# Kernel tuning notes

Hardware: AMD Instinct MI355X
Metric: run time of the kernel (lower is better)

The kernel has to match this reference:

```python
import jax, jax.numpy as jnp
import numpy as np

L, N, M = 128, 512, 256   # batch-like dim, recurrence length, feature dim (M_size1)
TK, H = 4, 8              # num_blocks, num_heads
DH = M // H
EPS = 1e-5


def setup_inputs() -> dict:
    key = jax.random.key(0)
    ks = jax.random.split(key, 8)
    s = 0.05  # scale raw-randn params for numerical stability
    return {
        "x": jax.random.normal(ks[0], (L, N, M), jnp.float32),
        "weight": jax.random.normal(ks[1], (M, M), jnp.float32) * s,
        "Wqkv": jax.random.normal(ks[2], (TK, 3, H, DH, M), jnp.float32) * s,
        "Wo": jax.random.normal(ks[3], (TK, M, M), jnp.float32) * s,
        "ln_g": jnp.ones((M,), jnp.float32),
        "ln_b": jnp.zeros((M,), jnp.float32),
        "lnz_g": jnp.ones((M,), jnp.float32),
        "lnz_b": jnp.zeros((M,), jnp.float32),
        "fc1_w": jax.random.normal(ks[4], (4 * M, M), jnp.float32) / np.float32(np.sqrt(M)),
        "fc1_b": jnp.zeros((4 * M,), jnp.float32),
        "fc2_w": jax.random.normal(ks[5], (M, 4 * M), jnp.float32) / np.float32(np.sqrt(4 * M)),
        "fc2_b": jnp.zeros((M,), jnp.float32),
    }


def _ln(x, g, b):
    mu = x.mean(-1, keepdims=True)
    var = x.var(-1, keepdims=True)  # biased variance, as torch LayerNorm
    return (x - mu) * jax.lax.rsqrt(var + EPS) * g + b


def _pos_bias(dtype):
    # bias[j, z]   = sin(j / 10000**(2z/M)) for even z
    # bias[j, z+1] = cos(j / 10000**(2z/M))
    pos = jnp.arange(N, dtype=dtype)                      # j
    z = jnp.arange(0, M, 2, dtype=dtype)                  # even indices
    ang = pos[:, None] / (10000.0 ** (2.0 * z / M))       # (N, M/2)
    return jnp.stack([jnp.sin(ang), jnp.cos(ang)], axis=-1).reshape(N, M)


def reference(x, weight, Wqkv, Wo, ln_g, ln_b, lnz_g, lnz_b, fc1_w, fc1_b, fc2_w, fc2_b):
    # savespace: (L, N, M); positional bias depends only on (j, feature)
    s = jnp.einsum('lm,ijm->ijl', weight, x) + _pos_bias(x.dtype)[None]
    inv_sqrt_dh = np.float32(1.0 / np.sqrt(DH))
    for a in range(TK):
        qkv = jnp.einsum('xhdm,ijm->xijhd', Wqkv[a], _ln(s, ln_g, ln_b))
        q, k, v = qkv[0], qkv[1], qkv[2]                  # each (L, N, H, DH)
        rsa = jnp.einsum('ijhd,ijhd->ijh', q * inv_sqrt_dh, k)
        imv = rsa[..., None] * v                           # (L, N, H, DH)
        imv = jnp.cumsum(imv, axis=1)                      # retention recurrence over j
        s = jnp.einsum('nm,ijm->ijn', Wo[a], imv.reshape(L, N, M)) + s
        s = _ln(s, lnz_g, lnz_b) + s
        h = jax.nn.gelu(s @ fc1_w.T + fc1_b, approximate=False)
        s = h @ fc2_w.T + fc2_b
    return s
```

## Files before the change

kernel.cpp:

```cpp
#include <hip/hip_runtime.h>

typedef unsigned int u32;
typedef unsigned short u16;
typedef _Float16 f16;
typedef __attribute__((ext_vector_type(8))) _Float16 f16x8;
typedef __attribute__((ext_vector_type(4))) float f32x4;
typedef __attribute__((ext_vector_type(4))) u16 u16x4;

#define L_ 128
#define N_ 512
#define M_ 256
#define TK_ 4
#define H_ 8
#define R_ (L_*N_)
#define FF_ 1024

__device__ __forceinline__ u16 f2h(float v){ f16 h=(f16)v; return __builtin_bit_cast(u16,h); }
__device__ __forceinline__ float h2f(u16 b){ return (float)__builtin_bit_cast(f16,b); }
__device__ __forceinline__ f32x4 mfmah(f16x8 a, f16x8 b, f32x4 c){
  return __builtin_amdgcn_mfma_f32_16x16x32_f16(a,b,c,0,0,0);
}
__device__ __forceinline__ float gelu_f(float x){
  float e = __expf(-1.702f*x);
  float r = __builtin_amdgcn_rcpf(e + 1.f);
  return x*r;
}


__global__ void k_bias(float* __restrict__ bias){
  int j = blockIdx.x, l = threadIdx.x;
  int t = l>>1;
  float base = expf(-0.14391156831212757f * (float)t);
  float ang = (float)j * base;
  bias[j*M_ + l] = (l&1) ? cosf(ang) : sinf(ang);
}

__global__ void k_pack(const float* __restrict__ src, u16* __restrict__ dst, int K){
  int b = blockIdx.x; int nk = K>>6; int cg = b/nk, k64 = b%nk;
  int t = threadIdx.x;
  int st = t>>6, g = (t>>4)&3, lr = t&15;
  const float* sp = src + (cg*16+lr)*K + k64*64 + st*32 + g*8;
  f16x8 hv;
  #pragma unroll
  for (int e=0;e<8;e++) hv[e] = (f16)sp[e];
  *(f16x8*)(dst + b*1024 + t*8) = hv;
}

__global__ void k_pack_qkv(const float* __restrict__ w, u16* __restrict__ dst){
  int b = blockIdx.x;
  int a = b/192; int rmn = b%192; int grp = rmn>>2, k64 = rmn&3;
  int hd = grp/6, cidx = grp%6;
  int t = threadIdx.x;
  int st = t>>6, g = (t>>4)&3, lr = t&15;
  int cl = cidx*16 + lr;
  int x = cl>>5, d = cl&31;
  const float* sp = w + (((a*3+x)*H_+hd)*32 + d)*M_ + k64*64 + st*32 + g*8;
  f16x8 hv;
  #pragma unroll
  for (int e=0;e<8;e++) hv[e] = (f16)sp[e];
  *(f16x8*)(dst + b*1024 + t*8) = hv;
}

__device__ __forceinline__ void stageA16(const u16* __restrict__ src, u16* __restrict__ Abuf,
                                         int rowbase, int tid){
  int row = tid>>3, skh = tid&7;
  int k64 = skh>>1, st = skh&1;
  int rg = row>>4, lr = row&15;
  const u16* sp = src + (rowbase+row)*M_ + k64*64 + st*32;
  u16* dp = Abuf + (k64*4+rg)*1024 + st*512 + lr*8;
  #pragma unroll
  for (int gg=0;gg<4;gg++)
    *(uint4*)(dp + gg*128) = *(const uint4*)(sp + gg*8);
}

__global__ __launch_bounds__(512) void k_init(const float* __restrict__ X, const u16* __restrict__ Wf,
    const float* __restrict__ bias, const float* __restrict__ lg, const float* __restrict__ lb,
    float* __restrict__ out, u16* __restrict__ P1){
  __shared__ __align__(16) u16 Abuf[16*1024];
  __shared__ float zs[8][64][2];
  int tid = threadIdx.x;
  int wx = tid>>6, lane = tid&63;
  int g = lane>>4, lr = lane&15;
  int lo = g*128 + lr*8;
  int rowbase = blockIdx.x*64;
  {
    int row = tid>>3, skh = tid&7;
    int k64 = skh>>1, st = skh&1;
    int rg = row>>4, slr = row&15;
    const float* sp = X + (rowbase+row)*M_ + k64*64 + st*32;
    u16* dp = Abuf + (k64*4+rg)*1024 + st*512 + slr*8;
    #pragma unroll
    for (int gg=0;gg<4;gg++){
      f16x8 hv;
      #pragma unroll
      for (int e=0;e<8;e++) hv[e] = (f16)sp[gg*8+e];
      *(f16x8*)(dp + gg*128) = hv;
    }
  }
  __syncthreads();
  f32x4 acc[4][2];
  #pragma unroll
  for (int i=0;i<4;i++){ acc[i][0]=0.f; acc[i][1]=0.f; }
  #pragma unroll
  for (int k64=0;k64<4;k64++)
    #pragma unroll
    for (int st=0;st<2;st++){
      f16x8 a[4], b[2];
      #pragma unroll
      for (int i=0;i<4;i++) a[i] = *(const f16x8*)(Abuf + (k64*4 + i)*1024 + st*512 + lo);
      #pragma unroll
      for (int j=0;j<2;j++) b[j] = *(const f16x8*)(Wf + ((wx*2+j)*4 + k64)*1024 + st*512 + lo);
      #pragma unroll
      for (int i=0;i<4;i++)
        #pragma unroll
        for (int j=0;j<2;j++) acc[i][j] = mfmah(a[i], b[j], acc[i][j]);
    }
  #pragma unroll
  for (int i=0;i<4;i++)
    #pragma unroll
    for (int j=0;j<2;j++)
      #pragma unroll
      for (int r=0;r<4;r++){
        int row = rowbase + i*16 + g*4 + r;
        int col = wx*32 + j*16 + lr;
        acc[i][j][r] += bias[(row & (N_-1))*M_ + col];
        out[row*M_ + col] = acc[i][j][r];
      }
  #pragma unroll
  for (int i=0;i<4;i++)
    #pragma unroll
    for (int r=0;r<4;r++){
      float ps = 0.f, qs = 0.f;
      #pragma unroll
      for (int j=0;j<2;j++){ float t = acc[i][j][r]; ps += t; qs += t*t; }
      ps += __shfl_xor(ps,1); qs += __shfl_xor(qs,1);
      ps += __shfl_xor(ps,2); qs += __shfl_xor(qs,2);
      ps += __shfl_xor(ps,4); qs += __shfl_xor(qs,4);
      ps += __shfl_xor(ps,8); qs += __shfl_xor(qs,8);
      if (lr == 0){
        int rowl = i*16 + g*4 + r;
        zs[wx][rowl][0] = ps;
        zs[wx][rowl][1] = qs;
      }
    }
  __syncthreads();
  #pragma unroll
  for (int i=0;i<4;i++)
    #pragma unroll
    for (int r=0;r<4;r++){
      int rowl = i*16 + g*4 + r;
      float sum=0.f, sq=0.f;
      #pragma unroll
      for (int q=0;q<8;q++){ sum += zs[q][rowl][0]; sq += zs[q][rowl][1]; }
      float mean = sum*(1.f/M_);
      float var  = sq*(1.f/M_) - mean*mean;
      float rstd = rsqrtf(var + 1e-5f);
      int row = rowbase + rowl;
      #pragma unroll
      for (int j=0;j<2;j++){
        int col = wx*32 + j*16 + lr;
        P1[row*M_ + col] = f2h((acc[i][j][r]-mean)*rstd*lg[col] + lb[col]);
      }
    }
}

__global__ __launch_bounds__(512) void k_qkv(const u16* __restrict__ P1, const u16* __restrict__ Wq,
    u16* __restrict__ imv){
  __shared__ __align__(16) u16 Abuf[16*1024];
  int tid = threadIdx.x;
  int hd = tid>>6, lane = tid&63;
  int g = lane>>4, lr = lane&15;
  int lo = g*128 + lr*8;
  int rowbase = blockIdx.x*64;
  stageA16(P1, Abuf, rowbase, tid);
  __syncthreads();
  const u16* Wb = Wq + hd*6*4096;
  const float isd = 0.17677669529663687f;
  float rsa[4][4];
  {
    f32x4 aqk[4][4];
    #pragma unroll
    for (int i=0;i<4;i++)
      #pragma unroll
      for (int c=0;c<4;c++) aqk[i][c] = 0.f;
    #pragma unroll
    for (int k64=0;k64<4;k64++)
      #pragma unroll
      for (int st=0;st<2;st++){
        f16x8 a[4];
        #pragma unroll
        for (int i=0;i<4;i++) a[i] = *(const f16x8*)(Abuf + (k64*4 + i)*1024 + st*512 + lo);
        #pragma unroll
        for (int c=0;c<4;c++){
          f16x8 b = *(const f16x8*)(Wb + (c*4 + k64)*1024 + st*512 + lo);
          #pragma unroll
          for (int i=0;i<4;i++) aqk[i][c] = mfmah(a[i], b, aqk[i][c]);
        }
      }
    #pragma unroll
    for (int i=0;i<4;i++){
      f32x4 p = aqk[i][0]*aqk[i][2] + aqk[i][1]*aqk[i][3];
      #pragma unroll
      for (int r=0;r<4;r++){
        float v = p[r];
        v += __shfl_xor(v,1); v += __shfl_xor(v,2);
        v += __shfl_xor(v,4); v += __shfl_xor(v,8);
        rsa[i][r] = v * isd;
      }
    }
  }
  f32x4 av[4][2];
  #pragma unroll
  for (int i=0;i<4;i++){ av[i][0]=0.f; av[i][1]=0.f; }
  #pragma unroll
  for (int k64=0;k64<4;k64++)
    #pragma unroll
    for (int st=0;st<2;st++){
      f16x8 a[4];
      #pragma unroll
      for (int i=0;i<4;i++) a[i] = *(const f16x8*)(Abuf + (k64*4 + i)*1024 + st*512 + lo);
      #pragma unroll
      for (int c=0;c<2;c++){
        f16x8 b = *(const f16x8*)(Wb + ((4+c)*4 + k64)*1024 + st*512 + lo);
        #pragma unroll
        for (int i=0;i<4;i++) av[i][c] = mfmah(a[i], b, av[i][c]);
      }
    }
  #pragma unroll
  for (int i=0;i<4;i++)
    #pragma unroll
    for (int r=0;r<4;r++){
      int row = rowbase + i*16 + g*4 + r;
      imv[row*M_ + hd*32 + lr]      = f2h(rsa[i][r]*av[i][0][r]);
      imv[row*M_ + hd*32 + 16 + lr] = f2h(rsa[i][r]*av[i][1][r]);
    }
}

__global__ __launch_bounds__(256) void k_scan(const u16* __restrict__ imv, u16* __restrict__ P1){
  __shared__ float tot[4][64][2];
  const u32* s32 = (const u32*)imv;
  u32* d32 = (u32*)P1;
  int bi = blockIdx.x;
  int i = bi>>1, mc = bi&1;
  int tid = threadIdx.x;
  int ml = tid&63, jc = tid>>6;
  int base = i*(N_*M_/2) + jc*128*(M_/2) + mc*64 + ml;
  float a0 = 0.f, a1 = 0.f;
  for (int jb=0;jb<128;jb+=8){
    u32 t[8];
    #pragma unroll
    for (int u=0;u<8;u++) t[u] = s32[base + (jb+u)*(M_/2)];
    #pragma unroll
    for (int u=0;u<8;u++){ a0 += h2f((u16)(t[u]&0xffff)); a1 += h2f((u16)(t[u]>>16)); }
  }
  tot[jc][ml][0] = a0; tot[jc][ml][1] = a1;
  __syncthreads();
  float p0 = 0.f, p1 = 0.f;
  #pragma unroll
  for (int q=0;q<3;q++) if (q<jc){ p0 += tot[q][ml][0]; p1 += tot[q][ml][1]; }
  a0 = p0; a1 = p1;
  for (int jb=0;jb<128;jb+=8){
    u32 t[8];
    #pragma unroll
    for (int u=0;u<8;u++) t[u] = s32[base + (jb+u)*(M_/2)];
    #pragma unroll
    for (int u=0;u<8;u++){
      a0 += h2f((u16)(t[u]&0xffff));
      a1 += h2f((u16)(t[u]>>16));
      d32[base + (jb+u)*(M_/2)] = (u32)f2h(a0) | ((u32)f2h(a1)<<16);
    }
  }
}

__global__ __launch_bounds__(512) void k_wo(u16* __restrict__ P1, const u16* __restrict__ Wf,
    const float* __restrict__ sold, const float* __restrict__ lg, const float* __restrict__ lb){
  __shared__ __align__(16) u16 Abuf[16*1024];
  __shared__ float zs[8][64][2];
  int tid = threadIdx.x;
  int wx = tid>>6, lane = tid&63;
  int g = lane>>4, lr = lane&15;
  int lo = g*128 + lr*8;
  int rowbase = blockIdx.x*64;
  stageA16(P1, Abuf, rowbase, tid);
  __syncthreads();
  f32x4 acc[4][2];
  #pragma unroll
  for (int i=0;i<4;i++){ acc[i][0]=0.f; acc[i][1]=0.f; }
  #pragma unroll
  for (int k64=0;k64<4;k64++)
    #pragma unroll
    for (int st=0;st<2;st++){
      f16x8 a[4], b[2];
      #pragma unroll
      for (int i=0;i<4;i++) a[i] = *(const f16x8*)(Abuf + (k64*4 + i)*1024 + st*512 + lo);
      #pragma unroll
      for (int j=0;j<2;j++) b[j] = *(const f16x8*)(Wf + ((wx*2+j)*4 + k64)*1024 + st*512 + lo);
      #pragma unroll
      for (int i=0;i<4;i++)
        #pragma unroll
        for (int j=0;j<2;j++) acc[i][j] = mfmah(a[i], b[j], acc[i][j]);
    }
  #pragma unroll
  for (int i=0;i<4;i++)
    #pragma unroll
    for (int j=0;j<2;j++)
      #pragma unroll
      for (int r=0;r<4;r++){
        int row = rowbase + i*16 + g*4 + r;
        int col = wx*32 + j*16 + lr;
        acc[i][j][r] += sold[row*M_ + col];
      }
  #pragma unroll
  for (int i=0;i<4;i++)
    #pragma unroll
    for (int r=0;r<4;r++){
      float ps = 0.f, qs = 0.f;
      #pragma unroll
      for (int j=0;j<2;j++){ float t = acc[i][j][r]; ps += t; qs += t*t; }
      ps += __shfl_xor(ps,1); qs += __shfl_xor(qs,1);
      ps += __shfl_xor(ps,2); qs += __shfl_xor(qs,2);
      ps += __shfl_xor(ps,4); qs += __shfl_xor(qs,4);
      ps += __shfl_xor(ps,8); qs += __shfl_xor(qs,8);
      if (lr == 0){
        int rowl = i*16 + g*4 + r;
        zs[wx][rowl][0] = ps;
        zs[wx][rowl][1] = qs;
      }
    }
  __syncthreads();
  #pragma unroll
  for (int i=0;i<4;i++)
    #pragma unroll
    for (int r=0;r<4;r++){
      int rowl = i*16 + g*4 + r;
      float sum=0.f, sq=0.f;
      #pragma unroll
      for (int q=0;q<8;q++){ sum += zs[q][rowl][0]; sq += zs[q][rowl][1]; }
      float mean = sum*(1.f/M_);
      float var  = sq*(1.f/M_) - mean*mean;
      float rstd = rsqrtf(var + 1e-5f);
      int row = rowbase + rowl;
      #pragma unroll
      for (int j=0;j<2;j++){
        int col = wx*32 + j*16 + lr;
        float zv = acc[i][j][r];
        P1[row*M_ + col] = f2h((zv-mean)*rstd*lg[col] + lb[col] + zv);
      }
    }
}

__global__ __launch_bounds__(512) void k_fc(u16* __restrict__ P1,
    const u16* __restrict__ W1f, const float* __restrict__ b1,
    const u16* __restrict__ W2f, const float* __restrict__ b2,
    const float* __restrict__ lg, const float* __restrict__ lb,
    float* __restrict__ out){
  __shared__ __align__(16) u16 Abuf[16*1024];
  __shared__ __align__(16) u16 Hbuf[2][64*128];
  __shared__ float zs[8][64][2];
  int tid = threadIdx.x;
  int wx = tid>>6, lane = tid&63;
  int g = lane>>4, lr = lane&15;
  int lo = g*128 + lr*8;
  int rowbase = blockIdx.x*64;
  stageA16(P1, Abuf, rowbase, tid);
  __syncthreads();
  f32x4 acc2[4][2];
  #pragma unroll
  for (int i=0;i<4;i++){ acc2[i][0]=0.f; acc2[i][1]=0.f; }
  for (int c=0;c<8;c++){
    u16* Hb = Hbuf[c&1];
    f32x4 acc1[4];
    #pragma unroll
    for (int j=0;j<4;j++) acc1[j] = 0.f;
    #pragma unroll
    for (int k64=0;k64<4;k64++)
      #pragma unroll
      for (int st=0;st<2;st++){
        f16x8 aw = *(const f16x8*)(W1f + ((c*8 + wx)*4 + k64)*1024 + st*512 + lo);
        #pragma unroll
        for (int j=0;j<4;j++){
          f16x8 bs = *(const f16x8*)(Abuf + (k64*4 + j)*1024 + st*512 + lo);
          acc1[j] = mfmah(aw, bs, acc1[j]);
        }
      }
    {
      int fl = wx*16 + g*4;
      int kc = fl>>6, kloc = fl&63;
      float4 b1v = *(const float4*)(b1 + c*128 + fl);
      float bb[4] = {b1v.x, b1v.y, b1v.z, b1v.w};
      #pragma unroll
      for (int j=0;j<4;j++){
        int row = j*16 + lr;
        u16x4 hv;
        #pragma unroll
        for (int r=0;r<4;r++)
          hv[r] = f2h(gelu_f(acc1[j][r] + bb[r]));
        int phys = ((kloc>>3) ^ row) & 7;
        *(u16x4*)(Hb + row*128 + kc*64 + phys*8 + (kloc&7)) = hv;
      }
    }
    __syncthreads();
    #pragma unroll
    for (int kcl=0;kcl<2;kcl++)
      #pragma unroll
      for (int st=0;st<2;st++){
        f16x8 ah[4], bb2[2];
        #pragma unroll
        for (int j=0;j<2;j++)
          bb2[j] = *(const f16x8*)(W2f + ((wx*2+j)*16 + c*2 + kcl)*1024 + st*512 + lo);
        #pragma unroll
        for (int i=0;i<4;i++){
          int hrow = i*16 + lr;
          int phys = (((st<<2)|g) ^ hrow) & 7;
          ah[i] = *(const f16x8*)(Hb + hrow*128 + kcl*64 + phys*8);
        }
        #pragma unroll
        for (int i=0;i<4;i++)
          #pragma unroll
          for (int j=0;j<2;j++) acc2[i][j] = mfmah(ah[i], bb2[j], acc2[i][j]);
      }
  }
  #pragma unroll
  for (int i=0;i<4;i++)
    #pragma unroll
    for (int j=0;j<2;j++)
      #pragma unroll
      for (int r=0;r<4;r++){
        int row = rowbase + i*16 + g*4 + r;
        int col = wx*32 + j*16 + lr;
        acc2[i][j][r] += b2[col];
        out[row*M_ + col] = acc2[i][j][r];
      }
  #pragma unroll
  for (int i=0;i<4;i++)
    #pragma unroll
    for (int r=0;r<4;r++){
      float ps = 0.f, qs = 0.f;
      #pragma unroll
      for (int j=0;j<2;j++){ float t = acc2[i][j][r]; ps += t; qs += t*t; }
      ps += __shfl_xor(ps,1); qs += __shfl_xor(qs,1);
      ps += __shfl_xor(ps,2); qs += __shfl_xor(qs,2);
      ps += __shfl_xor(ps,4); qs += __shfl_xor(qs,4);
      ps += __shfl_xor(ps,8); qs += __shfl_xor(qs,8);
      if (lr == 0){
        int rowl = i*16 + g*4 + r;
        zs[wx][rowl][0] = ps;
        zs[wx][rowl][1] = qs;
      }
    }
  __syncthreads();
  #pragma unroll
  for (int i=0;i<4;i++)
    #pragma unroll
    for (int r=0;r<4;r++){
      int rowl = i*16 + g*4 + r;
      float sum=0.f, sq=0.f;
      #pragma unroll
      for (int q=0;q<8;q++){ sum += zs[q][rowl][0]; sq += zs[q][rowl][1]; }
      float mean = sum*(1.f/M_);
      float var  = sq*(1.f/M_) - mean*mean;
      float rstd = rsqrtf(var + 1e-5f);
      int row = rowbase + rowl;
      #pragma unroll
      for (int j=0;j<2;j++){
        int col = wx*32 + j*16 + lr;
        P1[row*M_ + col] = f2h((acc2[i][j][r]-mean)*rstd*lg[col] + lb[col]);
      }
    }
}

extern "C" void kernel_launch(void* const* d_in, const int* in_sizes, int n_in,
                              void* d_out, int out_size, void* d_ws, size_t ws_size,
                              hipStream_t stream){
  const float* x      = (const float*)d_in[0];
  const float* weight = (const float*)d_in[1];
  const float* wqkv   = (const float*)d_in[2];
  const float* wo     = (const float*)d_in[3];
  const float* ln_g   = (const float*)d_in[4];
  const float* ln_b   = (const float*)d_in[5];
  const float* lnz_g  = (const float*)d_in[6];
  const float* lnz_b  = (const float*)d_in[7];
  const float* fc1_w  = (const float*)d_in[8];
  const float* fc1_b  = (const float*)d_in[9];
  const float* fc2_w  = (const float*)d_in[10];
  const float* fc2_b  = (const float*)d_in[11];
  float* out = (float*)d_out;
  char* ws = (char*)d_ws;
  size_t off = 0;
  u16* wqkvf   = (u16*)(ws + off); off += 1572864;
  u16* wof     = (u16*)(ws + off); off += 524288;
  u16* fc1f    = (u16*)(ws + off); off += 524288;
  u16* fc2f    = (u16*)(ws + off); off += 524288;
  u16* weightf = (u16*)(ws + off); off += 131072;
  float* bias  = (float*)(ws + off); off += 524288;
  u16* P1      = (u16*)(ws + off); off += 33554432;
  u16* imv     = (u16*)(ws + off); off += 33554432;

  k_bias<<<N_, M_, 0, stream>>>(bias);
  k_pack<<<64, 128, 0, stream>>>(weight, weightf, 256);
  k_pack_qkv<<<768, 128, 0, stream>>>(wqkv, wqkvf);
  k_pack<<<256, 128, 0, stream>>>(wo, wof, 256);
  k_pack<<<256, 128, 0, stream>>>(fc1_w, fc1f, 256);
  k_pack<<<256, 128, 0, stream>>>(fc2_w, fc2f, 1024);
  k_init<<<R_/64, 512, 0, stream>>>(x, weightf, bias, ln_g, ln_b, out, P1);
  for (int a=0; a<TK_; a++){
    k_qkv<<<R_/64, 512, 0, stream>>>(P1, wqkvf + a*196608, imv);
    k_scan<<<L_*2, 256, 0, stream>>>(imv, P1);
    k_wo<<<R_/64, 512, 0, stream>>>(P1, wof + a*65536, out, lnz_g, lnz_b);
    k_fc<<<R_/64, 512, 0, stream>>>(P1, fc1f, fc1_b, fc2f, fc2_b, ln_g, ln_b, out);
  }
}
```

Baseline: 793.3 us.

## Store residual stream in fp16, pad LDS tiles, skip final-layer LayerNorm

The residual stream s is now kept in an fp16 workspace buffer instead of the fp32 output, which halves the global traffic for its writes and reads between kernels. Only the last fc kernel writes fp32 to out. That kernel also drops the LayerNorm epilogue, whose result nothing downstream uses. The LDS A-tile strides are padded (1044/520 instead of 1024/512) to reduce bank conflicts. Bias and packed weight buffers now alias the imv workspace. The fp16 residual adds rounding error that can build up across the four blocks.

```diff
diff --git a/kernel.cpp b/kernel.cpp
--- a/kernel.cpp
+++ b/kernel.cpp
@@ -14,6 +14,8 @@
 #define H_ 8
 #define R_ (L_*N_)
 #define FF_ 1024
+#define FS 1044
+#define HS 520
 
 __device__ __forceinline__ u16 f2h(float v){ f16 h=(f16)v; return __builtin_bit_cast(u16,h); }
 __device__ __forceinline__ float h2f(u16 b){ return (float)__builtin_bit_cast(f16,b); }
@@ -67,7 +69,7 @@
   int k64 = skh>>1, st = skh&1;
   int rg = row>>4, lr = row&15;
   const u16* sp = src + (rowbase+row)*M_ + k64*64 + st*32;
-  u16* dp = Abuf + (k64*4+rg)*1024 + st*512 + lr*8;
+  u16* dp = Abuf + (k64*4+rg)*FS + st*HS + lr*8;
   #pragma unroll
   for (int gg=0;gg<4;gg++)
     *(uint4*)(dp + gg*128) = *(const uint4*)(sp + gg*8);
@@ -75,8 +77,8 @@
 
 __global__ __launch_bounds__(512) void k_init(const float* __restrict__ X, const u16* __restrict__ Wf,
     const float* __restrict__ bias, const float* __restrict__ lg, const float* __restrict__ lb,
-    float* __restrict__ out, u16* __restrict__ P1){
-  __shared__ __align__(16) u16 Abuf[16*1024];
+    u16* __restrict__ s16, u16* __restrict__ P1){
+  __shared__ __align__(16) u16 Abuf[16*FS];
   __shared__ float zs[8][64][2];
   int tid = threadIdx.x;
   int wx = tid>>6, lane = tid&63;
@@ -88,7 +90,7 @@
     int k64 = skh>>1, st = skh&1;
     int rg = row>>4, slr = row&15;
     const float* sp = X + (rowbase+row)*M_ + k64*64 + st*32;
-    u16* dp = Abuf + (k64*4+rg)*1024 + st*512 + slr*8;
+    u16* dp = Abuf + (k64*4+rg)*FS + st*HS + slr*8;
     #pragma unroll
     for (int gg=0;gg<4;gg++){
       f16x8 hv;
@@ -107,7 +109,7 @@
     for (int st=0;st<2;st++){
       f16x8 a[4], b[2];
       #pragma unroll
-      for (int i=0;i<4;i++) a[i] = *(const f16x8*)(Abuf + (k64*4 + i)*1024 + st*512 + lo);
+      for (int i=0;i<4;i++) a[i] = *(const f16x8*)(Abuf + (k64*4 + i)*FS + st*HS + lo);
       #pragma unroll
       for (int j=0;j<2;j++) b[j] = *(const f16x8*)(Wf + ((wx*2+j)*4 + k64)*1024 + st*512 + lo);
       #pragma unroll
@@ -124,7 +126,7 @@
         int row = rowbase + i*16 + g*4 + r;
         int col = wx*32 + j*16 + lr;
         acc[i][j][r] += bias[(row & (N_-1))*M_ + col];
-        out[row*M_ + col] = acc[i][j][r];
+        s16[row*M_ + col] = f2h(acc[i][j][r]);
       }
   #pragma unroll
   for (int i=0;i<4;i++)
@@ -166,7 +168,7 @@
 
 __global__ __launch_bounds__(512) void k_qkv(const u16* __restrict__ P1, const u16* __restrict__ Wq,
     u16* __restrict__ imv){
-  __shared__ __align__(16) u16 Abuf[16*1024];
+  __shared__ __align__(16) u16 Abuf[16*FS];
   int tid = threadIdx.x;
   int hd = tid>>6, lane = tid&63;
   int g = lane>>4, lr = lane&15;
@@ -189,7 +191,7 @@
       for (int st=0;st<2;st++){
         f16x8 a[4];
         #pragma unroll
-        for (int i=0;i<4;i++) a[i] = *(const f16x8*)(Abuf + (k64*4 + i)*1024 + st*512 + lo);
+        for (int i=0;i<4;i++) a[i] = *(const f16x8*)(Abuf + (k64*4 + i)*FS + st*HS + lo);
         #pragma unroll
         for (int c=0;c<4;c++){
           f16x8 b = *(const f16x8*)(Wb + (c*4 + k64)*1024 + st*512 + lo);
@@ -218,7 +220,7 @@
     for (int st=0;st<2;st++){
       f16x8 a[4];
       #pragma unroll
-      for (int i=0;i<4;i++) a[i] = *(const f16x8*)(Abuf + (k64*4 + i)*1024 + st*512 + lo);
+      for (int i=0;i<4;i++) a[i] = *(const f16x8*)(Abuf + (k64*4 + i)*FS + st*HS + lo);
       #pragma unroll
       for (int c=0;c<2;c++){
         f16x8 b = *(const f16x8*)(Wb + ((4+c)*4 + k64)*1024 + st*512 + lo);
@@ -273,8 +275,8 @@
 }
 
 __global__ __launch_bounds__(512) void k_wo(u16* __restrict__ P1, const u16* __restrict__ Wf,
-    const float* __restrict__ sold, const float* __restrict__ lg, const float* __restrict__ lb){
-  __shared__ __align__(16) u16 Abuf[16*1024];
+    const u16* __restrict__ s16, const float* __restrict__ lg, const float* __restrict__ lb){
+  __shared__ __align__(16) u16 Abuf[16*FS];
   __shared__ float zs[8][64][2];
   int tid = threadIdx.x;
   int wx = tid>>6, lane = tid&63;
@@ -292,7 +294,7 @@
     for (int st=0;st<2;st++){
       f16x8 a[4], b[2];
       #pragma unroll
-      for (int i=0;i<4;i++) a[i] = *(const f16x8*)(Abuf + (k64*4 + i)*1024 + st*512 + lo);
+      for (int i=0;i<4;i++) a[i] = *(const f16x8*)(Abuf + (k64*4 + i)*FS + st*HS + lo);
       #pragma unroll
       for (int j=0;j<2;j++) b[j] = *(const f16x8*)(Wf + ((wx*2+j)*4 + k64)*1024 + st*512 + lo);
       #pragma unroll
@@ -308,7 +310,7 @@
       for (int r=0;r<4;r++){
         int row = rowbase + i*16 + g*4 + r;
         int col = wx*32 + j*16 + lr;
-        acc[i][j][r] += sold[row*M_ + col];
+        acc[i][j][r] += h2f(s16[row*M_ + col]);
       }
   #pragma unroll
   for (int i=0;i<4;i++)
@@ -349,12 +351,13 @@
     }
 }
 
+template<int LAST>
 __global__ __launch_bounds__(512) void k_fc(u16* __restrict__ P1,
     const u16* __restrict__ W1f, const float* __restrict__ b1,
     const u16* __restrict__ W2f, const float* __restrict__ b2,
     const float* __restrict__ lg, const float* __restrict__ lb,
-    float* __restrict__ out){
-  __shared__ __align__(16) u16 Abuf[16*1024];
+    u16* __restrict__ s16, float* __restrict__ out){
+  __shared__ __align__(16) u16 Abuf[16*FS];
   __shared__ __align__(16) u16 Hbuf[2][64*128];
   __shared__ float zs[8][64][2];
   int tid = threadIdx.x;
@@ -379,7 +382,7 @@
         f16x8 aw = *(const f16x8*)(W1f + ((c*8 + wx)*4 + k64)*1024 + st*512 + lo);
         #pragma unroll
         for (int j=0;j<4;j++){
-          f16x8 bs = *(const f16x8*)(Abuf + (k64*4 + j)*1024 + st*512 + lo);
+          f16x8 bs = *(const f16x8*)(Abuf + (k64*4 + j)*FS + st*HS + lo);
           acc1[j] = mfmah(aw, bs, acc1[j]);
         }
       }
@@ -429,44 +432,47 @@
         int row = rowbase + i*16 + g*4 + r;
         int col = wx*32 + j*16 + lr;
         acc2[i][j][r] += b2[col];
-        out[row*M_ + col] = acc2[i][j][r];
-      }
-  #pragma unroll
-  for (int i=0;i<4;i++)
-    #pragma unroll
-    for (int r=0;r<4;r++){
-      float ps = 0.f, qs = 0.f;
-      #pragma unroll
-      for (int j=0;j<2;j++){ float t = acc2[i][j][r]; ps += t; qs += t*t; }
-      ps += __shfl_xor(ps,1); qs += __shfl_xor(qs,1);
-      ps += __shfl_xor(ps,2); qs += __shfl_xor(qs,2);
-      ps += __shfl_xor(ps,4); qs += __shfl_xor(qs,4);
-      ps += __shfl_xor(ps,8); qs += __shfl_xor(qs,8);
-      if (lr == 0){
+        if (LAST) out[row*M_ + col] = acc2[i][j][r];
+        else      s16[row*M_ + col] = f2h(acc2[i][j][r]);
+      }
+  if (!LAST){
+    #pragma unroll
+    for (int i=0;i<4;i++)
+      #pragma unroll
+      for (int r=0;r<4;r++){
+        float ps = 0.f, qs = 0.f;
+        #pragma unroll
+        for (int j=0;j<2;j++){ float t = acc2[i][j][r]; ps += t; qs += t*t; }
+        ps += __shfl_xor(ps,1); qs += __shfl_xor(qs,1);
+        ps += __shfl_xor(ps,2); qs += __shfl_xor(qs,2);
+        ps += __shfl_xor(ps,4); qs += __shfl_xor(qs,4);
+        ps += __shfl_xor(ps,8); qs += __shfl_xor(qs,8);
+        if (lr == 0){
+          int rowl = i*16 + g*4 + r;
+          zs[wx][rowl][0] = ps;
+          zs[wx][rowl][1] = qs;
+        }
+      }
+    __syncthreads();
+    #pragma unroll
+    for (int i=0;i<4;i++)
+      #pragma unroll
+      for (int r=0;r<4;r++){
         int rowl = i*16 + g*4 + r;
-        zs[wx][rowl][0] = ps;
-        zs[wx][rowl][1] = qs;
-      }
-    }
-  __syncthreads();
-  #pragma unroll
-  for (int i=0;i<4;i++)
-    #pragma unroll
-    for (int r=0;r<4;r++){
-      int rowl = i*16 + g*4 + r;
-      float sum=0.f, sq=0.f;
-      #pragma unroll
-      for (int q=0;q<8;q++){ sum += zs[q][rowl][0]; sq += zs[q][rowl][1]; }
-      float mean = sum*(1.f/M_);
-      float var  = sq*(1.f/M_) - mean*mean;
-      float rstd = rsqrtf(var + 1e-5f);
-      int row = rowbase + rowl;
-      #pragma unroll
-      for (int j=0;j<2;j++){
-        int col = wx*32 + j*16 + lr;
-        P1[row*M_ + col] = f2h((acc2[i][j][r]-mean)*rstd*lg[col] + lb[col]);
-      }
-    }
+        float sum=0.f, sq=0.f;
+        #pragma unroll
+        for (int q=0;q<8;q++){ sum += zs[q][rowl][0]; sq += zs[q][rowl][1]; }
+        float mean = sum*(1.f/M_);
+        float var  = sq*(1.f/M_) - mean*mean;
+        float rstd = rsqrtf(var + 1e-5f);
+        int row = rowbase + rowl;
+        #pragma unroll
+        for (int j=0;j<2;j++){
+          int col = wx*32 + j*16 + lr;
+          P1[row*M_ + col] = f2h((acc2[i][j][r]-mean)*rstd*lg[col] + lb[col]);
+        }
+      }
+  }
 }
 
 extern "C" void kernel_launch(void* const* d_in, const int* in_sizes, int n_in,
@@ -487,14 +493,15 @@
   float* out = (float*)d_out;
   char* ws = (char*)d_ws;
   size_t off = 0;
-  u16* wqkvf   = (u16*)(ws + off); off += 1572864;
-  u16* wof     = (u16*)(ws + off); off += 524288;
-  u16* fc1f    = (u16*)(ws + off); off += 524288;
-  u16* fc2f    = (u16*)(ws + off); off += 524288;
-  u16* weightf = (u16*)(ws + off); off += 131072;
-  float* bias  = (float*)(ws + off); off += 524288;
-  u16* P1      = (u16*)(ws + off); off += 33554432;
-  u16* imv     = (u16*)(ws + off); off += 33554432;
+  u16* wqkvf = (u16*)(ws + off); off += 1572864;
+  u16* wof   = (u16*)(ws + off); off += 524288;
+  u16* fc1f  = (u16*)(ws + off); off += 524288;
+  u16* fc2f  = (u16*)(ws + off); off += 524288;
+  u16* P1    = (u16*)(ws + off); off += 33554432;
+  u16* imv   = (u16*)(ws + off); off += 33554432;
+  u16* s16   = (u16*)(ws + off); off += 33554432;
+  float* bias    = (float*)imv;
+  u16*   weightf = (u16*)((char*)imv + 524288);
 
   k_bias<<<N_, M_, 0, stream>>>(bias);
   k_pack<<<64, 128, 0, stream>>>(weight, weightf, 256);
@@ -502,11 +509,14 @@
   k_pack<<<256, 128, 0, stream>>>(wo, wof, 256);
   k_pack<<<256, 128, 0, stream>>>(fc1_w, fc1f, 256);
   k_pack<<<256, 128, 0, stream>>>(fc2_w, fc2f, 1024);
-  k_init<<<R_/64, 512, 0, stream>>>(x, weightf, bias, ln_g, ln_b, out, P1);
+  k_init<<<R_/64, 512, 0, stream>>>(x, weightf, bias, ln_g, ln_b, s16, P1);
   for (int a=0; a<TK_; a++){
     k_qkv<<<R_/64, 512, 0, stream>>>(P1, wqkvf + a*196608, imv);
     k_scan<<<L_*2, 256, 0, stream>>>(imv, P1);
-    k_wo<<<R_/64, 512, 0, stream>>>(P1, wof + a*65536, out, lnz_g, lnz_b);
-    k_fc<<<R_/64, 512, 0, stream>>>(P1, fc1f, fc1_b, fc2f, fc2_b, ln_g, ln_b, out);
-  }
-}
+    k_wo<<<R_/64, 512, 0, stream>>>(P1, wof + a*65536, s16, lnz_g, lnz_b);
+    if (a < TK_-1)
+      k_fc<0><<<R_/64, 512, 0, stream>>>(P1, fc1f, fc1_b, fc2f, fc2_b, ln_g, ln_b, s16, out);
+    else
+      k_fc<1><<<R_/64, 512, 0, stream>>>(P1, fc1f, fc1_b, fc2f, fc2_b, ln_g, ln_b, s16, out);
+  }
+}
```

Result: faster. 761.5 us (-4.0%).
